# Kernel optimization log

Hardware: AMD Instinct MI355X
Metric: run time of the kernel (lower is better)

## Reference

```python
import jax, jax.numpy as jnp
import numpy as np
import math

EMB = 2048
N_Q = 32
N_KV = 8
HEAD = EMB // N_Q  # 64
N_REP = N_Q // N_KV  # 4
B, T = 2, 2048
ROPE_BASE = 10000.0


def setup_inputs() -> dict:
    key = jax.random.key(0)
    ks = jax.random.split(key, 9)
    s = 0.02
    return {
        "x": jax.random.normal(ks[0], (B, T, EMB), jnp.float32),
        "Wq": jax.random.normal(ks[1], (EMB, EMB), jnp.float32) * s,
        "bq": jax.random.normal(ks[2], (EMB,), jnp.float32) * s,
        "Wk": jax.random.normal(ks[3], (EMB, N_KV * HEAD), jnp.float32) * s,
        "bk": jax.random.normal(ks[4], (N_KV * HEAD,), jnp.float32) * s,
        "Wv": jax.random.normal(ks[5], (EMB, N_KV * HEAD), jnp.float32) * s,
        "bv": jax.random.normal(ks[6], (N_KV * HEAD,), jnp.float32) * s,
        "Wo": jax.random.normal(ks[7], (EMB, EMB), jnp.float32) * s,
        "bo": jax.random.normal(ks[8], (EMB,), jnp.float32) * s,
    }


def _rope_cos_sin(t, dim, dtype):
    inv_freq = 1.0 / (ROPE_BASE ** (jnp.arange(0, dim, 2, dtype=jnp.float32) / dim))
    freqs = jnp.arange(t, dtype=jnp.float32)[:, None] * inv_freq[None, :]  # (T, D/2)
    emb = jnp.concatenate([freqs, freqs], axis=-1)  # (T, D)
    return jnp.cos(emb).astype(dtype), jnp.sin(emb).astype(dtype)


def _rotate_half(x):
    d = x.shape[-1] // 2
    return jnp.concatenate([-x[..., d:], x[..., :d]], axis=-1)


def reference(x, Wq, bq, Wk, bk, Wv, bv, Wo, bo):
    b, t, c = x.shape
    q = (x @ Wq + bq).reshape(b, t, N_Q, HEAD)
    k = (x @ Wk + bk).reshape(b, t, N_KV, HEAD)
    v = (x @ Wv + bv).reshape(b, t, N_KV, HEAD)

    cos, sin = _rope_cos_sin(t, HEAD, x.dtype)  # (T, HEAD)
    cos = cos[None, :, None, :]
    sin = sin[None, :, None, :]
    q = q * cos + _rotate_half(q) * sin
    k = k * cos + _rotate_half(k) * sin

    # (B, H, T, D)
    q = q.transpose(0, 2, 1, 3)
    k = k.transpose(0, 2, 1, 3)
    v = v.transpose(0, 2, 1, 3)

    # repeat_kv: expand kv heads to match query heads
    k = jnp.repeat(k, N_REP, axis=1)
    v = jnp.repeat(v, N_REP, axis=1)

    scale = 1.0 / math.sqrt(HEAD)
    att = jnp.einsum("bhqd,bhkd->bhqk", q, k) * scale
    causal = jnp.tril(jnp.ones((t, t), dtype=bool))
    att = jnp.where(causal[None, None], att, jnp.finfo(att.dtype).min)
    att = jax.nn.softmax(att, axis=-1)

    y = jnp.einsum("bhqk,bhkd->bhqd", att, v)
    y = y.transpose(0, 2, 1, 3).reshape(b, t, c)
    return y @ Wo + bo
```

## Files before the change

### kernel.cpp

```cpp
#include <hip/hip_runtime.h>
#include <hip/hip_bf16.h>
#include <cstdint>
#include <cstddef>

typedef __attribute__((ext_vector_type(4))) float f32x4;
typedef __attribute__((ext_vector_type(8))) short bf16x8;

#define B_    2
#define T_    2048
#define EMB_  2048
#define NQ_   32
#define NKV_  8
#define HEAD_ 64
#define NTOT_ 3072
#define M_    (B_ * T_)
#define QBLK_ 64
#define NK_   32

#define MFMA_ __builtin_amdgcn_mfma_f32_16x16x32_bf16

__device__ __forceinline__ unsigned short f2bf(float f) {
  union { float f; unsigned int u; } v; v.f = f;
  unsigned int r = v.u + 0x7fffu + ((v.u >> 16) & 1u);
  return (unsigned short)(r >> 16);
}

__device__ __forceinline__ float bf2f(unsigned short u) {
  union { unsigned int u; float f; } v; v.u = (unsigned int)u << 16; return v.f;
}

__device__ __forceinline__ unsigned int pk_bf16(float lo, float hi) {
  __hip_bfloat162 h = __float22bfloat162_rn(make_float2(lo, hi));
  union { __hip_bfloat162 h; unsigned int u; } c; c.h = h;
  return c.u;
}

__device__ __forceinline__ float ex2(float x) {
  float r;
  asm("v_exp_f32 %0, %1" : "=v"(r) : "v"(x));
  return r;
}

__device__ __forceinline__ void gload_lds16(const void* g, void* l) {
  __builtin_amdgcn_global_load_lds(
      (const __attribute__((address_space(1))) void*)g,
      (__attribute__((address_space(3))) void*)l, 16, 0, 0);
}

#define L2_10000 13.2877123795494f
#define QSCALE_  0.18033688011112043f

__global__ void prep_all_kernel(const float* __restrict__ x,
                                const float* __restrict__ Wq,
                                const float* __restrict__ Wk,
                                const float* __restrict__ Wv,
                                const float* __restrict__ Wo,
                                const float* __restrict__ bq,
                                const float* __restrict__ bk,
                                const float* __restrict__ bv,
                                unsigned short* __restrict__ xb,
                                unsigned short* __restrict__ WqkvT,
                                unsigned short* __restrict__ WoT,
                                float* __restrict__ bcat,
                                float2* __restrict__ cstab) {
  __shared__ float tile[32][33];
  const int bid = blockIdx.x;
  if (bid < 8192) {
    const int i = bid * 256 + threadIdx.x;
    float4 v = ((const float4*)x)[i];
    unsigned long long pk =
        (unsigned long long)f2bf(v.x) |
        ((unsigned long long)f2bf(v.y) << 16) |
        ((unsigned long long)f2bf(v.z) << 32) |
        ((unsigned long long)f2bf(v.w) << 48);
    *(unsigned long long*)(xb + (size_t)i * 4) = pk;
    return;
  }
  if (bid < 18432) {
    const int wb = bid - 8192;
    const int tx = threadIdx.x & 31, ty = threadIdx.x >> 5;
    const float* src;
    unsigned short* dst;
    int C, local;
    if (wb < 4096)      { src = Wq; dst = WqkvT;                       C = 2048; local = wb; }
    else if (wb < 5120) { src = Wk; dst = WqkvT + (size_t)2048 * 2048; C = 512;  local = wb - 4096; }
    else if (wb < 6144) { src = Wv; dst = WqkvT + (size_t)2560 * 2048; C = 512;  local = wb - 5120; }
    else                { src = Wo; dst = WoT;                         C = 2048; local = wb - 6144; }
    const int tilesx = C >> 5;
    const int c0 = (local % tilesx) * 32, r0 = (local / tilesx) * 32;
#pragma unroll
    for (int k = 0; k < 4; ++k)
      tile[ty + 8 * k][tx] = src[(size_t)(r0 + ty + 8 * k) * C + c0 + tx];
    __syncthreads();
#pragma unroll
    for (int k = 0; k < 4; ++k)
      dst[(size_t)(c0 + ty + 8 * k) * 2048 + r0 + tx] = f2bf(tile[tx][ty + 8 * k]);
    return;
  }
  if (bid == 18432) {
    const int t0 = threadIdx.x;
#pragma unroll
    for (int k = 0; k < 12; ++k) {
      const int i = k * 256 + t0;
      float v;
      if (i < 2048) v = bq[i];
      else if (i < 2560) v = bk[i - 2048];
      else v = bv[i - 2560];
      bcat[i] = v;
    }
    return;
  }
  {
    const int idx = (bid - 18433) * 256 + threadIdx.x;
    const int t = idx >> 5, i = idx & 31;
    float invf = exp2f(-(float)i * (L2_10000 / 32.f));
    float ang = (float)t * invf;
    float s, c; sincosf(ang, &s, &c);
    cstab[idx] = make_float2(c, s);
  }
}

__global__ void rope_fused_kernel(const unsigned short* __restrict__ qkv,
                                  const float2* __restrict__ tab,
                                  unsigned short* __restrict__ Qh,
                                  unsigned short* __restrict__ Kh,
                                  unsigned short* __restrict__ Vt) {
  int idx = blockIdx.x * 256 + threadIdx.x;
  if (idx < 4194304) {
    int i  = idx & 31;
    int h  = (idx >> 5) & 31;
    int bt = idx >> 10;
    int t  = bt & (T_ - 1);
    int b  = bt >> 11;
    float2 cs = tab[(t << 5) + i];
    const unsigned short* row = qkv + (size_t)bt * NTOT_ + h * 64;
    float x1 = bf2f(row[i]), x2 = bf2f(row[i + 32]);
    unsigned short* q = Qh + ((size_t)(b * NQ_ + h) * T_ + t) * HEAD_;
    q[i]      = f2bf((x1 * cs.x - x2 * cs.y) * QSCALE_);
    q[i + 32] = f2bf((x2 * cs.x + x1 * cs.y) * QSCALE_);
  } else if (idx < 5242880) {
    int j  = idx - 4194304;
    int i  = j & 31;
    int kh = (j >> 5) & 7;
    int bt = j >> 8;
    int t  = bt & (T_ - 1);
    int b  = bt >> 11;
    float2 cs = tab[(t << 5) + i];
    const unsigned short* row = qkv + (size_t)bt * NTOT_ + 2048 + kh * 64;
    float x1 = bf2f(row[i]), x2 = bf2f(row[i + 32]);
    unsigned short* kp = Kh + ((size_t)(b * NKV_ + kh) * T_ + t) * HEAD_;
    kp[i]      = f2bf(x1 * cs.x - x2 * cs.y);
    kp[i + 32] = f2bf(x2 * cs.x + x1 * cs.y);
  } else {
    int j  = idx - 5242880;
    int t  = j & (T_ - 1);
    int d  = (j >> 11) & 63;
    int kh = (j >> 17) & 7;
    int b  = j >> 20;
    Vt[((size_t)((b * NKV_ + kh) * 64 + d)) * T_ + t] =
        qkv[(size_t)(b * T_ + t) * NTOT_ + 2560 + kh * 64 + d];
  }
}


__launch_bounds__(512, 4)
__global__ void gemm_qkv_3ph(const unsigned short* __restrict__ A,
                             const unsigned short* __restrict__ BT,
                             const float* __restrict__ bias,
                             unsigned short* __restrict__ C) {
  __shared__ unsigned short sh[2 * 20480];
  const int tid = threadIdx.x;
  const int lane = tid & 63, l16 = lane & 15, lg = lane >> 4;
  const int wave = tid >> 6, wm = wave >> 2, wn = wave & 3;
  const int bid = blockIdx.x;
  const int sw = (bid & 7) * 64 + (bid >> 3);
  const int mt = sw & 31, nt = sw >> 5;
  const int m0 = mt * 128, n0 = nt * 192;
  const int arow = tid >> 3;
  const int usrc = (tid & 7) ^ (arow & 7);
  const int swz = l16 & 7;
  const int uo0 = (lg ^ swz) << 3;
  const int uo1 = ((4 + lg) ^ swz) << 3;

  f32x4 acc[4][3];
#pragma unroll
  for (int i = 0; i < 4; ++i)
#pragma unroll
    for (int j = 0; j < 3; ++j) acc[i][j] = (f32x4){0.f, 0.f, 0.f, 0.f};

  auto STG = [&](int u) {
    if (u >= 5 * NK_) return;
    const int kt = u / 5, j = u % 5;
    char* bufb = (char*)sh + (kt & 1) * 40960;
    if (j < 2) {
      gload_lds16(A + (size_t)(m0 + j * 64 + arow) * 2048 + kt * 64 + usrc * 8,
                  bufb + j * 8192 + tid * 16);
    } else {
      const int jj = j - 2;
      gload_lds16(BT + (size_t)(n0 + jj * 64 + arow) * 2048 + kt * 64 + usrc * 8,
                  bufb + 16384 + jj * 8192 + tid * 16);
    }
  };

#pragma unroll
  for (int u = 0; u < 7; ++u) STG(u);
  asm volatile("s_waitcnt vmcnt(2)" ::: "memory");
  __builtin_amdgcn_s_barrier();

  for (int t = 0; t < NK_; ++t) {
    const unsigned short* Ab = sh + (t & 1) * 20480;
    const unsigned short* Bb = Ab + 8192;

    bf16x8 af[4][2], bfr[2];
#pragma unroll
    for (int fi = 0; fi < 4; ++fi) {
      const int ro = (fi * 32 + wm * 16 + l16) * 64;
      af[fi][0] = *(const bf16x8*)(Ab + ro + uo0);
      af[fi][1] = *(const bf16x8*)(Ab + ro + uo1);
    }
    {
      const int ro = (wn * 16 + l16) * 64;
      bfr[0] = *(const bf16x8*)(Bb + ro + uo0);
      bfr[1] = *(const bf16x8*)(Bb + ro + uo1);
    }
    STG(7 + 5 * t);  STG(8 + 5 * t);
    __builtin_amdgcn_s_barrier();
    asm volatile("s_waitcnt lgkmcnt(0)" ::: "memory");
    __builtin_amdgcn_sched_barrier(0);
    __builtin_amdgcn_s_setprio(1);
#pragma unroll
    for (int fi = 0; fi < 4; ++fi) {
      acc[fi][0] = MFMA_(af[fi][0], bfr[0], acc[fi][0], 0, 0, 0);
      acc[fi][0] = MFMA_(af[fi][1], bfr[1], acc[fi][0], 0, 0, 0);
    }
    __builtin_amdgcn_s_setprio(0);
    __builtin_amdgcn_s_barrier();

    {
      const int ro = (64 + wn * 16 + l16) * 64;
      bfr[0] = *(const bf16x8*)(Bb + ro + uo0);
      bfr[1] = *(const bf16x8*)(Bb + ro + uo1);
    }
    STG(9 + 5 * t);  STG(10 + 5 * t);
    __builtin_amdgcn_s_barrier();
    asm volatile("s_waitcnt lgkmcnt(0)" ::: "memory");
    __builtin_amdgcn_sched_barrier(0);
    __builtin_amdgcn_s_setprio(1);
#pragma unroll
    for (int fi = 0; fi < 4; ++fi) {
      acc[fi][1] = MFMA_(af[fi][0], bfr[0], acc[fi][1], 0, 0, 0);
      acc[fi][1] = MFMA_(af[fi][1], bfr[1], acc[fi][1], 0, 0, 0);
    }
    __builtin_amdgcn_s_setprio(0);
    __builtin_amdgcn_s_barrier();

    {
      const int ro = (128 + wn * 16 + l16) * 64;
      bfr[0] = *(const bf16x8*)(Bb + ro + uo0);
      bfr[1] = *(const bf16x8*)(Bb + ro + uo1);
    }
    STG(11 + 5 * t);
    __builtin_amdgcn_s_barrier();
    asm volatile("s_waitcnt lgkmcnt(0)" ::: "memory");
    __builtin_amdgcn_sched_barrier(0);
    __builtin_amdgcn_s_setprio(1);
#pragma unroll
    for (int fi = 0; fi < 4; ++fi) {
      acc[fi][2] = MFMA_(af[fi][0], bfr[0], acc[fi][2], 0, 0, 0);
      acc[fi][2] = MFMA_(af[fi][1], bfr[1], acc[fi][2], 0, 0, 0);
    }
    __builtin_amdgcn_s_setprio(0);
    if (t < NK_ - 2)       asm volatile("s_waitcnt vmcnt(2)" ::: "memory");
    else if (t == NK_ - 2) asm volatile("s_waitcnt vmcnt(0)" ::: "memory");
    __builtin_amdgcn_s_barrier();
  }

#pragma unroll
  for (int fj = 0; fj < 3; ++fj) {
    const int col = n0 + fj * 64 + wn * 16 + l16;
    const float bv = bias[col];
#pragma unroll
    for (int fi = 0; fi < 4; ++fi) {
      const int row0 = m0 + fi * 32 + wm * 16 + lg * 4;
#pragma unroll
      for (int r = 0; r < 4; ++r)
        C[(size_t)(row0 + r) * NTOT_ + col] = f2bf(acc[fi][fj][r] + bv);
    }
  }
}


__launch_bounds__(512, 2)
__global__ void gemm_o_2ph(const unsigned short* __restrict__ A,
                           const unsigned short* __restrict__ BT,
                           const float* __restrict__ bias,
                           float* __restrict__ C) {
  __shared__ unsigned short sh[2 * 24576];
  const int tid = threadIdx.x;
  const int lane = tid & 63, l16 = lane & 15, lg = lane >> 4;
  const int wave = tid >> 6, wm = wave >> 2, wn = wave & 3;
  const int bid = blockIdx.x;
  const int sw = (bid & 7) * 32 + (bid >> 3);
  const int mt = sw & 31, nt = sw >> 5;
  const int m0 = mt * 128, n0 = nt * 256;
  const int arow = tid >> 3;
  const int usrc = (tid & 7) ^ (arow & 7);
  const int swz = l16 & 7;
  const int uo0 = (lg ^ swz) << 3;
  const int uo1 = ((4 + lg) ^ swz) << 3;

  f32x4 acc[4][4];
#pragma unroll
  for (int i = 0; i < 4; ++i)
#pragma unroll
    for (int j = 0; j < 4; ++j) acc[i][j] = (f32x4){0.f, 0.f, 0.f, 0.f};

  auto STG = [&](int u) {
    if (u >= 6 * NK_) return;
    const int kt = u / 6, j = u % 6;
    char* bufb = (char*)sh + (kt & 1) * 49152;
    if (j < 2) {
      gload_lds16(A + (size_t)(m0 + j * 64 + arow) * 2048 + kt * 64 + usrc * 8,
                  bufb + j * 8192 + tid * 16);
    } else {
      const int jj = j - 2;
      gload_lds16(BT + (size_t)(n0 + jj * 64 + arow) * 2048 + kt * 64 + usrc * 8,
                  bufb + 16384 + jj * 8192 + tid * 16);
    }
  };

#pragma unroll
  for (int u = 0; u < 9; ++u) STG(u);
  asm volatile("s_waitcnt vmcnt(3)" ::: "memory");
  __builtin_amdgcn_s_barrier();

  for (int t = 0; t < NK_; ++t) {
    const unsigned short* Ab = sh + (t & 1) * 24576;
    const unsigned short* Bb = Ab + 8192;

    bf16x8 af[4][2], bfr[2][2];
#pragma unroll
    for (int fi = 0; fi < 4; ++fi) {
      const int ro = (fi * 32 + wm * 16 + l16) * 64;
      af[fi][0] = *(const bf16x8*)(Ab + ro + uo0);
      af[fi][1] = *(const bf16x8*)(Ab + ro + uo1);
    }
#pragma unroll
    for (int fj = 0; fj < 2; ++fj) {
      const int ro = (fj * 64 + wn * 16 + l16) * 64;
      bfr[fj][0] = *(const bf16x8*)(Bb + ro + uo0);
      bfr[fj][1] = *(const bf16x8*)(Bb + ro + uo1);
    }
    STG(9 + 6 * t);  STG(10 + 6 * t);  STG(11 + 6 * t);
    __builtin_amdgcn_s_barrier();
    asm volatile("s_waitcnt lgkmcnt(0)" ::: "memory");
    __builtin_amdgcn_sched_barrier(0);
    __builtin_amdgcn_s_setprio(1);
#pragma unroll
    for (int fi = 0; fi < 4; ++fi)
#pragma unroll
      for (int fj = 0; fj < 2; ++fj) {
        acc[fi][fj] = MFMA_(af[fi][0], bfr[fj][0], acc[fi][fj], 0, 0, 0);
        acc[fi][fj] = MFMA_(af[fi][1], bfr[fj][1], acc[fi][fj], 0, 0, 0);
      }
    __builtin_amdgcn_s_setprio(0);
    __builtin_amdgcn_s_barrier();

#pragma unroll
    for (int fj = 0; fj < 2; ++fj) {
      const int ro = ((2 + fj) * 64 + wn * 16 + l16) * 64;
      bfr[fj][0] = *(const bf16x8*)(Bb + ro + uo0);
      bfr[fj][1] = *(const bf16x8*)(Bb + ro + uo1);
    }
    STG(12 + 6 * t);  STG(13 + 6 * t);  STG(14 + 6 * t);
    __builtin_amdgcn_s_barrier();
    asm volatile("s_waitcnt lgkmcnt(0)" ::: "memory");
    __builtin_amdgcn_sched_barrier(0);
    __builtin_amdgcn_s_setprio(1);
#pragma unroll
    for (int fi = 0; fi < 4; ++fi)
#pragma unroll
      for (int fj = 0; fj < 2; ++fj) {
        acc[fi][2 + fj] = MFMA_(af[fi][0], bfr[fj][0], acc[fi][2 + fj], 0, 0, 0);
        acc[fi][2 + fj] = MFMA_(af[fi][1], bfr[fj][1], acc[fi][2 + fj], 0, 0, 0);
      }
    __builtin_amdgcn_s_setprio(0);
    if (t < NK_ - 2)       asm volatile("s_waitcnt vmcnt(3)" ::: "memory");
    else if (t == NK_ - 2) asm volatile("s_waitcnt vmcnt(0)" ::: "memory");
    __builtin_amdgcn_s_barrier();
  }

#pragma unroll
  for (int fj = 0; fj < 4; ++fj) {
    const int col = n0 + fj * 64 + wn * 16 + l16;
    const float bv = bias[col];
#pragma unroll
    for (int fi = 0; fi < 4; ++fi) {
      const int row0 = m0 + fi * 32 + wm * 16 + lg * 4;
#pragma unroll
      for (int r = 0; r < 4; ++r)
        C[(size_t)(row0 + r) * EMB_ + col] = acc[fi][fj][r] + bv;
    }
  }
}


__launch_bounds__(256, 2)
__global__ void flash_attn_kernel(const unsigned short* __restrict__ Qh,
                                  const unsigned short* __restrict__ Kh,
                                  const unsigned short* __restrict__ Vt,
                                  unsigned short* __restrict__ Y) {
  __shared__ unsigned short Klds[2][64 * 64];
  __shared__ unsigned short Vlds[2][64 * 64];
  __shared__ unsigned short Plds[4][16 * 64];
  const int tid = threadIdx.x;
  const int wave = tid >> 6, lane = tid & 63;
  const int l16 = lane & 15, lg = lane >> 4;
  const int h = blockIdx.y, b = blockIdx.z;
  const int kh = h >> 2;

  const size_t kbase = (size_t)(b * NKV_ + kh) * T_ * HEAD_;
  const size_t vbase = (size_t)(b * NKV_ + kh) * HEAD_ * T_;
  const int srow = tid >> 3;
  const int csrc = (tid & 7) ^ (srow & 7);
  unsigned short* pl = Plds[wave];
  const f32x4 zero4 = {0.f, 0.f, 0.f, 0.f};
  const short one_bf = (short)0x3F80;
  const bf16x8 onesv = {one_bf, one_bf, one_bf, one_bf,
                        one_bf, one_bf, one_bf, one_bf};

#define STAGE(bi, kv0) do {                                                         \
    gload_lds16(Kh + kbase + (size_t)((kv0) + srow) * HEAD_ + csrc * 8,             \
                (char*)Klds[bi] + tid * 16);                                        \
    gload_lds16(Kh + kbase + (size_t)((kv0) + srow + 32) * HEAD_ + csrc * 8,        \
                (char*)Klds[bi] + 4096 + tid * 16);                                 \
    gload_lds16(Vt + vbase + (size_t)srow * T_ + (kv0) + csrc * 8,                  \
                (char*)Vlds[bi] + tid * 16);                                        \
    gload_lds16(Vt + vbase + (size_t)(srow + 32) * T_ + (kv0) + csrc * 8,           \
                (char*)Vlds[bi] + 4096 + tid * 16);                                 \
  } while (0)

  for (int seg = 0; seg < 2; ++seg) {
    const int qt = seg ? (31 - (int)blockIdx.x) : (int)blockIdx.x;
    const int q0 = qt * QBLK_;
    const int nt = qt + 1;

    bf16x8 aq0, aq1;
    {
      const unsigned short* qp =
          Qh + ((size_t)(b * NQ_ + h) * T_ + q0 + wave * 16 + l16) * HEAD_;
      aq0 = *(const bf16x8*)(qp + lg * 8);
      aq1 = *(const bf16x8*)(qp + 32 + lg * 8);
    }

    f32x4 oacc[4];
    f32x4 lsum = zero4;
#pragma unroll
    for (int df = 0; df < 4; ++df) oacc[df] = zero4;
    float mreg = -1e30f;

    STAGE(0, 0);

    for (int t = 0; t < nt; ++t) {
      if (t + 1 < nt) {
        STAGE((t + 1) & 1, (t + 1) * 64);
        asm volatile("s_waitcnt vmcnt(8)" ::: "memory");
      } else {
        asm volatile("s_waitcnt vmcnt(0)" ::: "memory");
      }
      __builtin_amdgcn_s_barrier();
      __builtin_amdgcn_sched_barrier(0);

      const unsigned short* Kb = Klds[t & 1];
      const unsigned short* Vb = Vlds[t & 1];
      const int kv0 = t * 64;

      float p[4][4];
#pragma unroll
      for (int cf = 0; cf < 4; ++cf) {
        const int krow = cf * 16 + l16;
        const bf16x8 k0 = *(const bf16x8*)(Kb + krow * 64 + ((lg ^ (krow & 7)) << 3));
        const bf16x8 k1 = *(const bf16x8*)(Kb + krow * 64 + (((4 + lg) ^ (krow & 7)) << 3));
        f32x4 z = zero4;
        z = MFMA_(k0, aq0, z, 0, 0, 0);
        z = MFMA_(k1, aq1, z, 0, 0, 0);
#pragma unroll
        for (int r = 0; r < 4; ++r) p[cf][r] = z[r];
      }

      if (t == nt - 1) {
        const int qg = q0 + wave * 16 + l16;
#pragma unroll
        for (int cf = 0; cf < 4; ++cf)
#pragma unroll
          for (int r = 0; r < 4; ++r)
            if (kv0 + cf * 16 + lg * 4 + r > qg) p[cf][r] = -1e30f;
      }

      float m = mreg;
#pragma unroll
      for (int cf = 0; cf < 4; ++cf) {
        m = fmaxf(m, fmaxf(p[cf][0], p[cf][1]));
        m = fmaxf(m, fmaxf(p[cf][2], p[cf][3]));
      }
      m = fmaxf(m, __shfl_xor(m, 16, 64));
      m = fmaxf(m, __shfl_xor(m, 32, 64));

      if (!__all(m - mreg <= 8.f)) {
        const float corr = ex2(mreg - m);
        mreg = m;
        lsum[0] *= corr;
#pragma unroll
        for (int df = 0; df < 4; ++df)
#pragma unroll
          for (int r = 0; r < 4; ++r) oacc[df][r] *= corr;
      }

#pragma unroll
      for (int cf = 0; cf < 4; ++cf)
#pragma unroll
        for (int r = 0; r < 4; ++r)
          p[cf][r] = ex2(p[cf][r] - mreg);

      const int row = l16;
#pragma unroll
      for (int cf = 0; cf < 4; ++cf) {
        const unsigned int w0 = pk_bf16(p[cf][0], p[cf][1]);
        const unsigned int w1 = pk_bf16(p[cf][2], p[cf][3]);
        const int u = cf * 2 + (lg >> 1);
        char* ad = (char*)pl + row * 128 + ((u ^ (row & 7)) << 4) + ((lg & 1) << 3);
        *(unsigned long long*)ad =
            (unsigned long long)w0 | ((unsigned long long)w1 << 32);
      }
      bf16x8 pf[2];
#pragma unroll
      for (int k2 = 0; k2 < 2; ++k2) {
        const int u = k2 * 4 + lg;
        pf[k2] = *(const bf16x8*)((char*)pl + row * 128 + ((u ^ (row & 7)) << 4));
      }

      lsum = MFMA_(onesv, pf[0], lsum, 0, 0, 0);
      lsum = MFMA_(onesv, pf[1], lsum, 0, 0, 0);
#pragma unroll
      for (int df = 0; df < 4; ++df) {
        const int vrow = df * 16 + l16;
        const bf16x8 v0 = *(const bf16x8*)(Vb + vrow * 64 + ((lg ^ (vrow & 7)) << 3));
        const bf16x8 v1 = *(const bf16x8*)(Vb + vrow * 64 + (((4 + lg) ^ (vrow & 7)) << 3));
        oacc[df] = MFMA_(v0, pf[0], oacc[df], 0, 0, 0);
        oacc[df] = MFMA_(v1, pf[1], oacc[df], 0, 0, 0);
      }

      asm volatile("s_waitcnt lgkmcnt(0)" ::: "memory");
      __builtin_amdgcn_sched_barrier(0);
      __builtin_amdgcn_s_barrier();
    }

    {
      const float inv = 1.f / lsum[0];
      const int tq = q0 + wave * 16 + l16;
      unsigned short* yp = Y + ((size_t)(b * T_ + tq)) * EMB_ + h * HEAD_;
#pragma unroll
      for (int df = 0; df < 4; ++df) {
        const unsigned int w0 = pk_bf16(oacc[df][0] * inv, oacc[df][1] * inv);
        const unsigned int w1 = pk_bf16(oacc[df][2] * inv, oacc[df][3] * inv);
        *(unsigned long long*)(yp + df * 16 + lg * 4) =
            (unsigned long long)w0 | ((unsigned long long)w1 << 32);
      }
    }
  }
#undef STAGE
}


extern "C" void kernel_launch(void* const* d_in, const int* in_sizes, int n_in,
                              void* d_out, int out_size, void* d_ws, size_t ws_size,
                              hipStream_t stream) {
  const float* x  = (const float*)d_in[0];
  const float* Wq = (const float*)d_in[1];
  const float* bq = (const float*)d_in[2];
  const float* Wk = (const float*)d_in[3];
  const float* bk = (const float*)d_in[4];
  const float* Wv = (const float*)d_in[5];
  const float* bv = (const float*)d_in[6];
  const float* Wo = (const float*)d_in[7];
  const float* bo = (const float*)d_in[8];
  float* out = (float*)d_out;

  char* ws = (char*)d_ws;
  size_t off = 0;
  auto alloc = [&](size_t bytes) {
    void* p = ws + off;
    off += (bytes + 255) & ~(size_t)255;
    return p;
  };
  unsigned short* xb     = (unsigned short*)alloc((size_t)M_ * EMB_ * 2);
  unsigned short* WqkvT  = (unsigned short*)alloc((size_t)NTOT_ * EMB_ * 2);
  unsigned short* WoT    = (unsigned short*)alloc((size_t)EMB_ * EMB_ * 2);
  float*          bcat   = (float*)alloc((size_t)NTOT_ * 4);
  float2*         cstab  = (float2*)alloc((size_t)T_ * 32 * 8);
  unsigned short* QKVlin = (unsigned short*)alloc((size_t)M_ * NTOT_ * 2);
  unsigned short* Qh     = (unsigned short*)alloc((size_t)B_ * NQ_ * T_ * HEAD_ * 2);
  unsigned short* Kh     = (unsigned short*)alloc((size_t)B_ * NKV_ * T_ * HEAD_ * 2);
  unsigned short* Vt     = (unsigned short*)alloc((size_t)B_ * NKV_ * HEAD_ * T_ * 2);
  unsigned short* Yb     = (unsigned short*)alloc((size_t)M_ * EMB_ * 2);

  prep_all_kernel<<<18689, 256, 0, stream>>>(x, Wq, Wk, Wv, Wo, bq, bk, bv,
                                             xb, WqkvT, WoT, bcat, cstab);

  gemm_qkv_3ph<<<512, 512, 0, stream>>>(xb, WqkvT, bcat, QKVlin);

  rope_fused_kernel<<<28672, 256, 0, stream>>>(QKVlin, cstab, Qh, Kh, Vt);

  flash_attn_kernel<<<dim3(16, NQ_, B_), 256, 0, stream>>>(Qh, Kh, Vt, Yb);

  gemm_o_2ph<<<256, 512, 0, stream>>>(Yb, WoT, bo, out);

  (void)in_sizes; (void)n_in; (void)out_size; (void)ws_size;
}
```

Before: 205.8 us.

## Fuse RoPE and head-layout scatter into QKV GEMM epilogue

The QKV projection GEMM now stages its biased bf16 output tile in shared memory, then applies RoPE and the Q scaling and scatters directly into the Qh, Kh and transposed Vt layouts. This removes the separate rope kernel launch and the round trip of the full QKV intermediate through global memory. The epilogue's global writes are scattered 2-byte stores (strided for Vt), which may be poorly coalesced, and the LDS staging adds a sync at the end of the GEMM.

```diff
diff --git a/kernel.cpp b/kernel.cpp
--- a/kernel.cpp
+++ b/kernel.cpp
@@ -120,54 +120,15 @@
   }
 }
 
-__global__ void rope_fused_kernel(const unsigned short* __restrict__ qkv,
-                                  const float2* __restrict__ tab,
-                                  unsigned short* __restrict__ Qh,
-                                  unsigned short* __restrict__ Kh,
-                                  unsigned short* __restrict__ Vt) {
-  int idx = blockIdx.x * 256 + threadIdx.x;
-  if (idx < 4194304) {
-    int i  = idx & 31;
-    int h  = (idx >> 5) & 31;
-    int bt = idx >> 10;
-    int t  = bt & (T_ - 1);
-    int b  = bt >> 11;
-    float2 cs = tab[(t << 5) + i];
-    const unsigned short* row = qkv + (size_t)bt * NTOT_ + h * 64;
-    float x1 = bf2f(row[i]), x2 = bf2f(row[i + 32]);
-    unsigned short* q = Qh + ((size_t)(b * NQ_ + h) * T_ + t) * HEAD_;
-    q[i]      = f2bf((x1 * cs.x - x2 * cs.y) * QSCALE_);
-    q[i + 32] = f2bf((x2 * cs.x + x1 * cs.y) * QSCALE_);
-  } else if (idx < 5242880) {
-    int j  = idx - 4194304;
-    int i  = j & 31;
-    int kh = (j >> 5) & 7;
-    int bt = j >> 8;
-    int t  = bt & (T_ - 1);
-    int b  = bt >> 11;
-    float2 cs = tab[(t << 5) + i];
-    const unsigned short* row = qkv + (size_t)bt * NTOT_ + 2048 + kh * 64;
-    float x1 = bf2f(row[i]), x2 = bf2f(row[i + 32]);
-    unsigned short* kp = Kh + ((size_t)(b * NKV_ + kh) * T_ + t) * HEAD_;
-    kp[i]      = f2bf(x1 * cs.x - x2 * cs.y);
-    kp[i + 32] = f2bf(x2 * cs.x + x1 * cs.y);
-  } else {
-    int j  = idx - 5242880;
-    int t  = j & (T_ - 1);
-    int d  = (j >> 11) & 63;
-    int kh = (j >> 17) & 7;
-    int b  = j >> 20;
-    Vt[((size_t)((b * NKV_ + kh) * 64 + d)) * T_ + t] =
-        qkv[(size_t)(b * T_ + t) * NTOT_ + 2560 + kh * 64 + d];
-  }
-}
-
 
 __launch_bounds__(512, 4)
 __global__ void gemm_qkv_3ph(const unsigned short* __restrict__ A,
                              const unsigned short* __restrict__ BT,
                              const float* __restrict__ bias,
-                             unsigned short* __restrict__ C) {
+                             const float2* __restrict__ cstab,
+                             unsigned short* __restrict__ Qh,
+                             unsigned short* __restrict__ Kh,
+                             unsigned short* __restrict__ Vt) {
   __shared__ unsigned short sh[2 * 20480];
   const int tid = threadIdx.x;
   const int lane = tid & 63, l16 = lane & 15, lg = lane >> 4;
@@ -275,16 +236,51 @@
     __builtin_amdgcn_s_barrier();
   }
 
-#pragma unroll
-  for (int fj = 0; fj < 3; ++fj) {
-    const int col = n0 + fj * 64 + wn * 16 + l16;
-    const float bv = bias[col];
-#pragma unroll
-    for (int fi = 0; fi < 4; ++fi) {
-      const int row0 = m0 + fi * 32 + wm * 16 + lg * 4;
-#pragma unroll
-      for (int r = 0; r < 4; ++r)
-        C[(size_t)(row0 + r) * NTOT_ + col] = f2bf(acc[fi][fj][r] + bv);
+  {
+    unsigned short* Clds = sh;
+#pragma unroll
+    for (int fj = 0; fj < 3; ++fj) {
+      const int col = fj * 64 + wn * 16 + l16;
+      const float bv = bias[n0 + col];
+#pragma unroll
+      for (int fi = 0; fi < 4; ++fi) {
+        const int row0 = fi * 32 + wm * 16 + lg * 4;
+#pragma unroll
+        for (int r = 0; r < 4; ++r)
+          Clds[(row0 + r) * 194 + col] = f2bf(acc[fi][fj][r] + bv);
+      }
+    }
+    __syncthreads();
+    const int row = tid & 127;
+    const int qq  = tid >> 7;
+    const int tg  = m0 + row;
+    const int b   = tg >> 11, tt = tg & 2047;
+#pragma unroll
+    for (int k = 0; k < 24; ++k) {
+      const int cidx = qq * 24 + k;
+      const int c  = (cidx >> 5) * 64 + (cidx & 31);
+      const int gc = n0 + c;
+      const int d  = cidx & 31;
+      const float x1 = bf2f(Clds[row * 194 + c]);
+      const float x2 = bf2f(Clds[row * 194 + c + 32]);
+      if (gc < 2048) {
+        const int h = gc >> 6;
+        const float2 cs = cstab[(tt << 5) + d];
+        unsigned short* qp = Qh + ((size_t)(b * NQ_ + h) * T_ + tt) * HEAD_ + d;
+        qp[0]  = f2bf((x1 * cs.x - x2 * cs.y) * QSCALE_);
+        qp[32] = f2bf((x2 * cs.x + x1 * cs.y) * QSCALE_);
+      } else if (gc < 2560) {
+        const int kh = (gc >> 6) - 32;
+        const float2 cs = cstab[(tt << 5) + d];
+        unsigned short* kp = Kh + ((size_t)(b * NKV_ + kh) * T_ + tt) * HEAD_ + d;
+        kp[0]  = f2bf(x1 * cs.x - x2 * cs.y);
+        kp[32] = f2bf(x2 * cs.x + x1 * cs.y);
+      } else {
+        const int kh = (gc >> 6) - 40;
+        unsigned short* vp = Vt + ((size_t)((b * NKV_ + kh) * 64 + d)) * T_ + tt;
+        vp[0]            = f2bf(x1);
+        vp[32 * (size_t)T_] = f2bf(x2);
+      }
     }
   }
 }
@@ -598,7 +594,6 @@
   unsigned short* WoT    = (unsigned short*)alloc((size_t)EMB_ * EMB_ * 2);
   float*          bcat   = (float*)alloc((size_t)NTOT_ * 4);
   float2*         cstab  = (float2*)alloc((size_t)T_ * 32 * 8);
-  unsigned short* QKVlin = (unsigned short*)alloc((size_t)M_ * NTOT_ * 2);
   unsigned short* Qh     = (unsigned short*)alloc((size_t)B_ * NQ_ * T_ * HEAD_ * 2);
   unsigned short* Kh     = (unsigned short*)alloc((size_t)B_ * NKV_ * T_ * HEAD_ * 2);
   unsigned short* Vt     = (unsigned short*)alloc((size_t)B_ * NKV_ * HEAD_ * T_ * 2);
@@ -607,9 +602,7 @@
   prep_all_kernel<<<18689, 256, 0, stream>>>(x, Wq, Wk, Wv, Wo, bq, bk, bv,
                                              xb, WqkvT, WoT, bcat, cstab);
 
-  gemm_qkv_3ph<<<512, 512, 0, stream>>>(xb, WqkvT, bcat, QKVlin);
-
-  rope_fused_kernel<<<28672, 256, 0, stream>>>(QKVlin, cstab, Qh, Kh, Vt);
+  gemm_qkv_3ph<<<512, 512, 0, stream>>>(xb, WqkvT, bcat, cstab, Qh, Kh, Vt);
 
   flash_attn_kernel<<<dim3(16, NQ_, B_), 256, 0, stream>>>(Qh, Kh, Vt, Yb);
 
```

After: 245.3 us. 1.19x slower.
